# Optimization experiments

Hardware: AMD Instinct MI355X
Metric: run time of the kernel (lower is better)

## Reference

```python
import jax, jax.numpy as jnp
import numpy as np

NUM_HEADS = 8
ATTENTION_SPAN = 128
LOOKAHEAD = True
NEG_INF = -1e9  # tf.keras Softmax mask adder


def setup_inputs() -> dict:
    key = jax.random.key(0)
    k1, k2, k3 = jax.random.split(key, 3)
    B, S, D = 4, 2048, 512
    x = jax.random.normal(k1, (B, S, D), dtype=jnp.float32)
    w_qkv = jax.random.normal(k2, (D, 3 * D), dtype=jnp.float32) * (D ** -0.5)
    w_proj = jax.random.normal(k3, (D, D), dtype=jnp.float32) * (D ** -0.5)
    return {"x": x, "w_qkv": w_qkv, "w_proj": w_proj}


def _band_mask(S: int) -> jnp.ndarray:
    idx = jnp.arange(S)
    m = jnp.abs(idx[None, :] - idx[:, None]) <= ATTENTION_SPAN
    if not LOOKAHEAD:
        m = m & (idx[None, :] <= idx[:, None])
    return m  # [S, S] bool


def reference(x, w_qkv, w_proj):
    B, S, D = x.shape
    H = NUM_HEADS
    hd = D // H
    scale = D ** -0.5  # NOTE: source scales by full dim, not head_dim

    qkv = x @ w_qkv                                   # [B,S,3D]
    qkv = qkv.reshape(B, S, H, 3 * hd).transpose(0, 2, 1, 3)  # [B,H,S,3hd]
    q, k, v = jnp.split(qkv, 3, axis=-1)              # each [B,H,S,hd]

    scores = jnp.einsum('bhqd,bhkd->bhqk', q, k) * scale  # [B,H,S,S]
    mask = _band_mask(S)[None, None, :, :]
    scores = scores + (1.0 - mask.astype(scores.dtype)) * NEG_INF
    attn = jax.nn.softmax(scores, axis=-1)

    out = jnp.einsum('bhqk,bhkd->bhqd', attn, v)      # [B,H,S,hd]
    out = out.transpose(0, 2, 1, 3).reshape(B, S, D)
    return out @ w_proj
```

## Files before the change

### kernel.cpp

```cpp
#include <hip/hip_runtime.h>

typedef unsigned short u16;
typedef __attribute__((ext_vector_type(8))) short s16x8;
typedef __attribute__((ext_vector_type(4))) float f32x4;

#define MFMA16(a, b, c) __builtin_amdgcn_mfma_f32_16x16x32_bf16((a), (b), (c), 0, 0, 0)

__device__ __forceinline__ u16 f2bf(float f) {
  unsigned u = __float_as_uint(f);
  u += 0x7fffu + ((u >> 16) & 1u);
  return (u16)(u >> 16);
}

__device__ __forceinline__ void gld_lds16(const void* g, void* l) {
  __builtin_amdgcn_global_load_lds(
      (const __attribute__((address_space(1))) void*)g,
      (__attribute__((address_space(3))) void*)l, 16, 0, 0);
}

__global__ __launch_bounds__(256) void xcast(const float* __restrict__ X,
                                             u16* __restrict__ Xb) {
  size_t idx = (size_t)blockIdx.x * 256 + threadIdx.x;
  const float4 f0 = *(const float4*)(X + idx * 8);
  const float4 f1 = *(const float4*)(X + idx * 8 + 4);
  float fs[8] = {f0.x, f0.y, f0.z, f0.w, f1.x, f1.y, f1.z, f1.w};
  s16x8 hv;
#pragma unroll
  for (int j = 0; j < 8; ++j) hv[j] = (short)f2bf(fs[j]);
  *(s16x8*)(Xb + idx * 8) = hv;
}

template <int PERM>
__global__ __launch_bounds__(256) void wcastT(const float* __restrict__ W, int K, int N,
                                              u16* __restrict__ T) {
  int idx = blockIdx.x * 256 + threadIdx.x;
  int total = N * (K >> 3);
  if (idx >= total) return;
  int n = idx % N;
  int kc = idx / N;
  int src_c;
  if (PERM) {
    int t = n >> 9, ct = n & 511, h = ct >> 6, d = ct & 63;
    src_c = h * 192 + t * 64 + d;
  } else {
    src_c = n;
  }
  s16x8 hv;
#pragma unroll
  for (int i = 0; i < 8; ++i) hv[i] = (short)f2bf(W[(size_t)(kc * 8 + i) * N + src_c]);
  *(s16x8*)(T + (size_t)n * K + (size_t)kc * 8) = hv;
}

template <int EPI, int NCOL>
__global__ __launch_bounds__(256) void gemm_bf16(
    const u16* __restrict__ A, const u16* __restrict__ B,
    float* __restrict__ OUT,
    u16* __restrict__ qo, u16* __restrict__ ko, u16* __restrict__ vto) {
  __shared__ u16 LDS[EPI ? 16640 : 16384];
  u16* SA = LDS;
  u16* SB = LDS + 8192;
  const int tid = threadIdx.x;
  const int w = tid >> 6, lane = tid & 63;
  const int l15 = lane & 15, l4 = lane >> 4;
  const int bid0 = blockIdx.x;
  const int work = (bid0 & 7) * (8 * NCOL) + (bid0 >> 3);
  const int bx = work / NCOL;
  const int by = work % NCOL;
  const int row0 = bx * 128;
  const int col0 = by * 128;
  const int wr = w >> 1, wc = w & 1;

  const int lrow = lane >> 3, lslot = lane & 7;
  const int srcoff = lrow * 1024 + ((lslot ^ lrow) << 4);
  const char* pA = (const char*)A + (size_t)(row0 + w * 32) * 1024 + srcoff;
  const char* pB = (const char*)B + (size_t)(col0 + w * 32) * 1024 + srcoff;
  u16* sAw = SA + (w * 32) * 64;
  u16* sBw = SB + (w * 32) * 64;

  const f32x4 fz = {0.f, 0.f, 0.f, 0.f};
  f32x4 acc[4][4];
  for (int a = 0; a < 4; ++a)
    for (int b = 0; b < 4; ++b) acc[a][b] = fz;

  for (int t = 0; t < 8; ++t) {
    const size_t kb = (size_t)t * 128;
#pragma unroll
    for (int j = 0; j < 4; ++j) {
      gld_lds16(pA + j * 8192 + kb, sAw + j * 512);
      gld_lds16(pB + j * 8192 + kb, sBw + j * 512);
    }
    __syncthreads();
#pragma unroll
    for (int ks = 0; ks < 2; ++ks) {
      s16x8 af[4], bf[4];
#pragma unroll
      for (int mi = 0; mi < 4; ++mi) {
        const int r = wr * 64 + mi * 16 + l15;
        const int sl = (ks * 4 + l4) ^ (r & 7);
        af[mi] = *(const s16x8*)&SA[r * 64 + sl * 8];
      }
#pragma unroll
      for (int nj = 0; nj < 4; ++nj) {
        const int r = wc * 64 + nj * 16 + l15;
        const int sl = (ks * 4 + l4) ^ (r & 7);
        bf[nj] = *(const s16x8*)&SB[r * 64 + sl * 8];
      }
#pragma unroll
      for (int nj = 0; nj < 4; ++nj)
#pragma unroll
        for (int mi = 0; mi < 4; ++mi) acc[mi][nj] = MFMA16(af[mi], bf[nj], acc[mi][nj]);
    }
    __syncthreads();
  }

  if (EPI == 0) {
#pragma unroll
    for (int mi = 0; mi < 4; ++mi)
#pragma unroll
      for (int nj = 0; nj < 4; ++nj)
#pragma unroll
        for (int rg = 0; rg < 4; ++rg) {
          int r_g = row0 + wr * 64 + mi * 16 + l4 * 4 + rg;
          int c_g = col0 + wc * 64 + nj * 16 + l15;
          OUT[(size_t)r_g * 512 + c_g] = acc[mi][nj][rg];
        }
    return;
  }

  const int b = row0 >> 11, srow = row0 & 2047;
  if (by < 8) {
    const int isq = (by < 4);
    const float QS = 0.06375874f;
    u16* dst = isq ? qo : ko;
#pragma unroll
    for (int mi = 0; mi < 4; ++mi)
#pragma unroll
      for (int nj = 0; nj < 4; ++nj)
#pragma unroll
        for (int rg = 0; rg < 4; ++rg) {
          float v = acc[mi][nj][rg];
          if (isq) v *= QS;
          int s = srow + wr * 64 + mi * 16 + l4 * 4 + rg;
          int ct = ((by & 3) * 128 + wc * 64 + nj * 16 + l15);
          int h = ct >> 6, d = ct & 63;
          dst[(((size_t)b * 8 + h) * 2048 + s) * 64 + d] = f2bf(v);
        }
  } else {
#pragma unroll
    for (int mi = 0; mi < 4; ++mi)
#pragma unroll
      for (int nj = 0; nj < 4; ++nj)
#pragma unroll
        for (int rg = 0; rg < 4; ++rg) {
          int c = wc * 64 + nj * 16 + l15;
          int s = wr * 64 + mi * 16 + l4 * 4 + rg;
          LDS[c * 130 + s] = f2bf(acc[mi][nj][rg]);
        }
    __syncthreads();
    const unsigned* LDSw = (const unsigned*)LDS;
    int c = tid >> 1, sh = tid & 1;
    int ct = (by - 8) * 128 + c;
    int h = ct >> 6, d = ct & 63;
    size_t o = (((size_t)b * 8 + h) * 64 + d) * 2048 + srow + sh * 64;
    unsigned wbuf[32];
#pragma unroll
    for (int p = 0; p < 32; ++p) wbuf[p] = LDSw[c * 65 + sh * 32 + p];
#pragma unroll
    for (int j = 0; j < 8; ++j) {
      uint4 u = {wbuf[j * 4], wbuf[j * 4 + 1], wbuf[j * 4 + 2], wbuf[j * 4 + 3]};
      *(uint4*)(vto + o + j * 8) = u;
    }
  }
}

__global__ __launch_bounds__(256, 4) void attn_kernel(
    const u16* __restrict__ q, const u16* __restrict__ k,
    const u16* __restrict__ vt, u16* __restrict__ ao) {
  __shared__ u16 KT[2][64 * 64];
  __shared__ u16 VT[2][64 * 64];
  __shared__ u16 Ph[4][16 * 64];
  const int tid = threadIdx.x;
  const int w = tid >> 6, lane = tid & 63;
  const int l15 = lane & 15, l4 = lane >> 4;
  const int bid0 = blockIdx.x;
  const int bid = (bid0 & 7) * 128 + (bid0 >> 3);
  const int qt = bid & 31, hh = (bid >> 5) & 7, b = bid >> 8;
  const size_t base = (size_t)(b * 8 + hh) * 2048 * 64;
  const int q0 = qt * 64 + w * 16;

  s16x8 qf[2];
#pragma unroll
  for (int ks = 0; ks < 2; ++ks)
    qf[ks] = *(const s16x8*)(q + base + (size_t)(q0 + l15) * 64 + ks * 32 + l4 * 8);

  const f32x4 fz = {0.f, 0.f, 0.f, 0.f};
  f32x4 O[4];
  for (int nd = 0; nd < 4; ++nd) O[nd] = fz;
  float l_acc[4] = {0.f, 0.f, 0.f, 0.f};

  const int lrow = lane >> 3, lslot = lane & 7;
  const int swzb = (lslot ^ lrow) << 4;
  const char* pK = (const char*)(k + base) + (w * 16 + lrow) * 128 + swzb;
  const char* pV = (const char*)(vt + base) + (size_t)(w * 16 + lrow) * 4096 + swzb;
  u16* dK = &KT[0][0] + w * 1024;
  u16* dV = &VT[0][0] + w * 1024;

#define STAGE(c_, b_)                                              \
  do {                                                             \
    gld_lds16(pK + (c_)*8192,            dK + (b_)*4096);          \
    gld_lds16(pK + (c_)*8192 + 1024,     dK + (b_)*4096 + 512);    \
    gld_lds16(pV + (c_)*128,             dV + (b_)*4096);          \
    gld_lds16(pV + (c_)*128 + 8 * 4096,  dV + (b_)*4096 + 512);    \
  } while (0)

  const int c0 = qt - 2 < 0 ? 0 : qt - 2;
  const int c1 = qt + 2 > 31 ? 31 : qt + 2;

  STAGE(c0, 0);
  __syncthreads();

  for (int c = c0; c <= c1; ++c) {
    const int buf = (c - c0) & 1;
    if (c < c1) STAGE(c + 1, buf ^ 1);
    const int kb = c * 64;
    f32x4 S[4];
    for (int nj = 0; nj < 4; ++nj) S[nj] = fz;
#pragma unroll
    for (int nj = 0; nj < 4; ++nj) {
      const int r = nj * 16 + l15;
#pragma unroll
      for (int ks = 0; ks < 2; ++ks) {
        const int sl = (ks * 4 + l4) ^ (r & 7);
        s16x8 kf = *(const s16x8*)&KT[buf][r * 64 + sl * 8];
        S[nj] = MFMA16(qf[ks], kf, S[nj]);
      }
    }
    const bool needmask = (kb + 63 - q0 > 128) || (q0 + 15 - kb > 128);
#pragma unroll
    for (int nj = 0; nj < 4; ++nj)
#pragma unroll
      for (int rg = 0; rg < 4; ++rg) {
        const int row = l4 * 4 + rg;
        const int col = nj * 16 + l15;
        float p = exp2f(S[nj][rg]);
        if (needmask) {
          int dd = (kb + col) - (q0 + row);
          if (dd > 128 || dd < -128) p = 0.f;
        }
        l_acc[rg] += p;
        const int e = (((col >> 3) ^ (row & 7)) << 3) + (col & 7);
        Ph[w][row * 64 + e] = f2bf(p);
      }
#pragma unroll
    for (int ksp = 0; ksp < 2; ++ksp) {
      const int sl0 = (ksp * 4 + l4) ^ (l15 & 7);
      s16x8 pa = *(const s16x8*)&Ph[w][l15 * 64 + sl0 * 8];
#pragma unroll
      for (int nd = 0; nd < 4; ++nd) {
        const int r = nd * 16 + l15;
        const int sl = (ksp * 4 + l4) ^ (r & 7);
        s16x8 vf = *(const s16x8*)&VT[buf][r * 64 + sl * 8];
        O[nd] = MFMA16(pa, vf, O[nd]);
      }
    }
    __syncthreads();
  }
#undef STAGE

#pragma unroll
  for (int rg = 0; rg < 4; ++rg) {
    float s = l_acc[rg];
    s += __shfl_xor(s, 1);
    s += __shfl_xor(s, 2);
    s += __shfl_xor(s, 4);
    s += __shfl_xor(s, 8);
    l_acc[rg] = 1.0f / s;
  }
#pragma unroll
  for (int rg = 0; rg < 4; ++rg) {
    const int s_g = q0 + l4 * 4 + rg;
#pragma unroll
    for (int nd = 0; nd < 4; ++nd) {
      float v = O[nd][rg] * l_acc[rg];
      const int c_g = hh * 64 + nd * 16 + l15;
      ao[((size_t)b * 2048 + s_g) * 512 + c_g] = f2bf(v);
    }
  }
}

extern "C" void kernel_launch(void* const* d_in, const int* in_sizes, int n_in,
                              void* d_out, int out_size, void* d_ws, size_t ws_size,
                              hipStream_t stream) {
  const float* x = (const float*)d_in[0];
  const float* wqkv = (const float*)d_in[1];
  const float* wproj = (const float*)d_in[2];
  float* out = (float*)d_out;

  char* ws = (char*)d_ws;
  size_t off = 0;
  auto alloc = [&](size_t bytes) {
    void* p = ws + off;
    off += (bytes + 255) & ~(size_t)255;
    return p;
  };
  const size_t E = (size_t)4 * 8 * 2048 * 64;
  u16* Xb  = (u16*)alloc(E * 2);
  u16* qb  = (u16*)alloc(E * 2);
  u16* kb  = (u16*)alloc(E * 2);
  u16* vtb = (u16*)alloc(E * 2);
  u16* aob = (u16*)alloc(E * 2);
  u16* wqT = (u16*)alloc((size_t)1536 * 512 * 2);
  u16* wpT = (u16*)alloc((size_t)512 * 512 * 2);

  xcast<<<dim3(2048), dim3(256), 0, stream>>>(x, Xb);
  wcastT<1><<<dim3(384), dim3(256), 0, stream>>>(wqkv, 512, 1536, wqT);
  wcastT<0><<<dim3(128), dim3(256), 0, stream>>>(wproj, 512, 512, wpT);
  gemm_bf16<1, 12><<<dim3(768), dim3(256), 0, stream>>>(Xb, wqT, nullptr, qb, kb, vtb);
  attn_kernel<<<dim3(1024), dim3(256), 0, stream>>>(qb, kb, vtb, aob);
  gemm_bf16<0, 4><<<dim3(256), dim3(256), 0, stream>>>(aob, wpT, out, nullptr, nullptr, nullptr);
}
```

Before: 73.42 us.

## Merge cast kernels into one launch and double attention query tile per block

The three fp32-to-bf16 cast kernels are folded into a single prep launch, cutting two kernel launches. The attention kernel now processes 128 queries per block with 8 waves, so each staged K/V tile is shared by twice as many waves and total K/V traffic drops. Waves also skip key tiles that lie entirely outside their band. The wider query tile spans 6 key chunks instead of 5, and blocks grow to 512 threads, which can change occupancy and add some idle waves per chunk.

```diff
diff --git a/kernel.cpp b/kernel.cpp
--- a/kernel.cpp
+++ b/kernel.cpp
@@ -18,37 +18,41 @@
       (__attribute__((address_space(3))) void*)l, 16, 0, 0);
 }
 
-__global__ __launch_bounds__(256) void xcast(const float* __restrict__ X,
-                                             u16* __restrict__ Xb) {
-  size_t idx = (size_t)blockIdx.x * 256 + threadIdx.x;
-  const float4 f0 = *(const float4*)(X + idx * 8);
-  const float4 f1 = *(const float4*)(X + idx * 8 + 4);
-  float fs[8] = {f0.x, f0.y, f0.z, f0.w, f1.x, f1.y, f1.z, f1.w};
-  s16x8 hv;
-#pragma unroll
-  for (int j = 0; j < 8; ++j) hv[j] = (short)f2bf(fs[j]);
-  *(s16x8*)(Xb + idx * 8) = hv;
-}
-
-template <int PERM>
-__global__ __launch_bounds__(256) void wcastT(const float* __restrict__ W, int K, int N,
-                                              u16* __restrict__ T) {
-  int idx = blockIdx.x * 256 + threadIdx.x;
-  int total = N * (K >> 3);
-  if (idx >= total) return;
-  int n = idx % N;
-  int kc = idx / N;
-  int src_c;
-  if (PERM) {
+__global__ __launch_bounds__(256) void prep(const float* __restrict__ X,
+                                            const float* __restrict__ Wqkv,
+                                            const float* __restrict__ Wproj,
+                                            u16* __restrict__ Xb,
+                                            u16* __restrict__ wqT,
+                                            u16* __restrict__ wpT) {
+  const int bid = blockIdx.x;
+  if (bid < 2048) {
+    size_t idx = (size_t)bid * 256 + threadIdx.x;
+    const float4 f0 = *(const float4*)(X + idx * 8);
+    const float4 f1 = *(const float4*)(X + idx * 8 + 4);
+    float fs[8] = {f0.x, f0.y, f0.z, f0.w, f1.x, f1.y, f1.z, f1.w};
+    s16x8 hv;
+#pragma unroll
+    for (int j = 0; j < 8; ++j) hv[j] = (short)f2bf(fs[j]);
+    *(s16x8*)(Xb + idx * 8) = hv;
+  } else if (bid < 2432) {
+    int idx = (bid - 2048) * 256 + threadIdx.x;
+    int n = idx % 1536;
+    int kc = idx / 1536;
     int t = n >> 9, ct = n & 511, h = ct >> 6, d = ct & 63;
-    src_c = h * 192 + t * 64 + d;
+    int src_c = h * 192 + t * 64 + d;
+    s16x8 hv;
+#pragma unroll
+    for (int i = 0; i < 8; ++i) hv[i] = (short)f2bf(Wqkv[(size_t)(kc * 8 + i) * 1536 + src_c]);
+    *(s16x8*)(wqT + (size_t)n * 512 + (size_t)kc * 8) = hv;
   } else {
-    src_c = n;
-  }
-  s16x8 hv;
-#pragma unroll
-  for (int i = 0; i < 8; ++i) hv[i] = (short)f2bf(W[(size_t)(kc * 8 + i) * N + src_c]);
-  *(s16x8*)(T + (size_t)n * K + (size_t)kc * 8) = hv;
+    int idx = (bid - 2432) * 256 + threadIdx.x;
+    int n = idx % 512;
+    int kc = idx / 512;
+    s16x8 hv;
+#pragma unroll
+    for (int i = 0; i < 8; ++i) hv[i] = (short)f2bf(Wproj[(size_t)(kc * 8 + i) * 512 + n]);
+    *(s16x8*)(wpT + (size_t)n * 512 + (size_t)kc * 8) = hv;
+  }
 }
 
 template <int EPI, int NCOL>
@@ -173,20 +177,20 @@
   }
 }
 
-__global__ __launch_bounds__(256, 4) void attn_kernel(
+__global__ __launch_bounds__(512, 6) void attn_kernel(
     const u16* __restrict__ q, const u16* __restrict__ k,
     const u16* __restrict__ vt, u16* __restrict__ ao) {
   __shared__ u16 KT[2][64 * 64];
   __shared__ u16 VT[2][64 * 64];
-  __shared__ u16 Ph[4][16 * 64];
+  __shared__ u16 Ph[8][16 * 64];
   const int tid = threadIdx.x;
   const int w = tid >> 6, lane = tid & 63;
   const int l15 = lane & 15, l4 = lane >> 4;
   const int bid0 = blockIdx.x;
-  const int bid = (bid0 & 7) * 128 + (bid0 >> 3);
-  const int qt = bid & 31, hh = (bid >> 5) & 7, b = bid >> 8;
+  const int bid = (bid0 & 7) * 64 + (bid0 >> 3);
+  const int qt = bid & 15, hh = (bid >> 4) & 7, b = bid >> 7;
   const size_t base = (size_t)(b * 8 + hh) * 2048 * 64;
-  const int q0 = qt * 64 + w * 16;
+  const int q0 = qt * 128 + w * 16;
 
   s16x8 qf[2];
 #pragma unroll
@@ -200,21 +204,19 @@
 
   const int lrow = lane >> 3, lslot = lane & 7;
   const int swzb = (lslot ^ lrow) << 4;
-  const char* pK = (const char*)(k + base) + (w * 16 + lrow) * 128 + swzb;
-  const char* pV = (const char*)(vt + base) + (size_t)(w * 16 + lrow) * 4096 + swzb;
-  u16* dK = &KT[0][0] + w * 1024;
-  u16* dV = &VT[0][0] + w * 1024;
-
-#define STAGE(c_, b_)                                              \
-  do {                                                             \
-    gld_lds16(pK + (c_)*8192,            dK + (b_)*4096);          \
-    gld_lds16(pK + (c_)*8192 + 1024,     dK + (b_)*4096 + 512);    \
-    gld_lds16(pV + (c_)*128,             dV + (b_)*4096);          \
-    gld_lds16(pV + (c_)*128 + 8 * 4096,  dV + (b_)*4096 + 512);    \
+  const char* pK = (const char*)(k + base) + (w * 8 + lrow) * 128 + swzb;
+  const char* pV = (const char*)(vt + base) + (size_t)(w * 8 + lrow) * 4096 + swzb;
+  u16* dK = &KT[0][0] + w * 512;
+  u16* dV = &VT[0][0] + w * 512;
+
+#define STAGE(c_, b_)                                    \
+  do {                                                   \
+    gld_lds16(pK + (c_) * 8192, dK + (b_) * 4096);       \
+    gld_lds16(pV + (c_) * 128,  dV + (b_) * 4096);       \
   } while (0)
 
-  const int c0 = qt - 2 < 0 ? 0 : qt - 2;
-  const int c1 = qt + 2 > 31 ? 31 : qt + 2;
+  const int c0 = (2 * qt - 2) < 0 ? 0 : (2 * qt - 2);
+  const int c1 = (2 * qt + 3) > 31 ? 31 : (2 * qt + 3);
 
   STAGE(c0, 0);
   __syncthreads();
@@ -223,44 +225,47 @@
     const int buf = (c - c0) & 1;
     if (c < c1) STAGE(c + 1, buf ^ 1);
     const int kb = c * 64;
-    f32x4 S[4];
-    for (int nj = 0; nj < 4; ++nj) S[nj] = fz;
-#pragma unroll
-    for (int nj = 0; nj < 4; ++nj) {
-      const int r = nj * 16 + l15;
-#pragma unroll
-      for (int ks = 0; ks < 2; ++ks) {
-        const int sl = (ks * 4 + l4) ^ (r & 7);
-        s16x8 kf = *(const s16x8*)&KT[buf][r * 64 + sl * 8];
-        S[nj] = MFMA16(qf[ks], kf, S[nj]);
+    const bool skip = (kb - (q0 + 15) > 128) || (q0 - (kb + 63) > 128);
+    if (!skip) {
+      f32x4 S[4];
+      for (int nj = 0; nj < 4; ++nj) S[nj] = fz;
+#pragma unroll
+      for (int nj = 0; nj < 4; ++nj) {
+        const int r = nj * 16 + l15;
+#pragma unroll
+        for (int ks = 0; ks < 2; ++ks) {
+          const int sl = (ks * 4 + l4) ^ (r & 7);
+          s16x8 kf = *(const s16x8*)&KT[buf][r * 64 + sl * 8];
+          S[nj] = MFMA16(qf[ks], kf, S[nj]);
+        }
       }
-    }
-    const bool needmask = (kb + 63 - q0 > 128) || (q0 + 15 - kb > 128);
-#pragma unroll
-    for (int nj = 0; nj < 4; ++nj)
-#pragma unroll
-      for (int rg = 0; rg < 4; ++rg) {
-        const int row = l4 * 4 + rg;
-        const int col = nj * 16 + l15;
-        float p = exp2f(S[nj][rg]);
-        if (needmask) {
-          int dd = (kb + col) - (q0 + row);
-          if (dd > 128 || dd < -128) p = 0.f;
-        }
-        l_acc[rg] += p;
-        const int e = (((col >> 3) ^ (row & 7)) << 3) + (col & 7);
-        Ph[w][row * 64 + e] = f2bf(p);
-      }
-#pragma unroll
-    for (int ksp = 0; ksp < 2; ++ksp) {
-      const int sl0 = (ksp * 4 + l4) ^ (l15 & 7);
-      s16x8 pa = *(const s16x8*)&Ph[w][l15 * 64 + sl0 * 8];
-#pragma unroll
-      for (int nd = 0; nd < 4; ++nd) {
-        const int r = nd * 16 + l15;
-        const int sl = (ksp * 4 + l4) ^ (r & 7);
-        s16x8 vf = *(const s16x8*)&VT[buf][r * 64 + sl * 8];
-        O[nd] = MFMA16(pa, vf, O[nd]);
+      const bool needmask = (kb + 63 - q0 > 128) || (q0 + 15 - kb > 128);
+#pragma unroll
+      for (int nj = 0; nj < 4; ++nj)
+#pragma unroll
+        for (int rg = 0; rg < 4; ++rg) {
+          const int row = l4 * 4 + rg;
+          const int col = nj * 16 + l15;
+          float p = exp2f(S[nj][rg]);
+          if (needmask) {
+            int dd = (kb + col) - (q0 + row);
+            if (dd > 128 || dd < -128) p = 0.f;
+          }
+          l_acc[rg] += p;
+          const int e = (((col >> 3) ^ (row & 7)) << 3) + (col & 7);
+          Ph[w][row * 64 + e] = f2bf(p);
+        }
+#pragma unroll
+      for (int ksp = 0; ksp < 2; ++ksp) {
+        const int sl0 = (ksp * 4 + l4) ^ (l15 & 7);
+        s16x8 pa = *(const s16x8*)&Ph[w][l15 * 64 + sl0 * 8];
+#pragma unroll
+        for (int nd = 0; nd < 4; ++nd) {
+          const int r = nd * 16 + l15;
+          const int sl = (ksp * 4 + l4) ^ (r & 7);
+          s16x8 vf = *(const s16x8*)&VT[buf][r * 64 + sl * 8];
+          O[nd] = MFMA16(pa, vf, O[nd]);
+        }
       }
     }
     __syncthreads();
@@ -312,10 +317,8 @@
   u16* wqT = (u16*)alloc((size_t)1536 * 512 * 2);
   u16* wpT = (u16*)alloc((size_t)512 * 512 * 2);
 
-  xcast<<<dim3(2048), dim3(256), 0, stream>>>(x, Xb);
-  wcastT<1><<<dim3(384), dim3(256), 0, stream>>>(wqkv, 512, 1536, wqT);
-  wcastT<0><<<dim3(128), dim3(256), 0, stream>>>(wproj, 512, 512, wpT);
+  prep<<<dim3(2560), dim3(256), 0, stream>>>(x, wqkv, wproj, Xb, wqT, wpT);
   gemm_bf16<1, 12><<<dim3(768), dim3(256), 0, stream>>>(Xb, wqT, nullptr, qb, kb, vtb);
-  attn_kernel<<<dim3(1024), dim3(256), 0, stream>>>(qb, kb, vtb, aob);
+  attn_kernel<<<dim3(512), dim3(512), 0, stream>>>(qb, kb, vtb, aob);
   gemm_bf16<0, 4><<<dim3(256), dim3(256), 0, stream>>>(aob, wpT, out, nullptr, nullptr, nullptr);
 }
```

New measurement: 70.42 us. 1.04x faster.
